# Kernel optimization log

Hardware: AMD Instinct MI355X
Metric: run time of the kernel (lower is better)

Reference implementation:

```python
import jax, jax.numpy as jnp
import numpy as np

N_NODES = 100_000
N_EDGES = 1_000_000
D_IN = 64
D_OUT = 64
N_TYPES = 16  # get_options().in_dim; must exceed gate types 9/11 referenced in source


def setup_inputs() -> dict:
    key = jax.random.key(0)
    k = jax.random.split(key, 6)
    feat = jax.random.normal(k[0], (N_NODES, D_IN), dtype=jnp.float32)
    src = jax.random.randint(k[1], (N_EDGES,), 0, N_NODES, dtype=jnp.int32)
    dst = jax.random.randint(k[2], (N_EDGES,), 0, N_NODES, dtype=jnp.int32)
    ntype2 = jax.random.randint(k[3], (N_NODES,), 0, N_TYPES, dtype=jnp.int32)
    # per-type Linear params; xavier-uniform-ish (gain=sqrt(2) for relu)
    limit = np.sqrt(2.0) * np.sqrt(6.0 / (D_IN + D_OUT))
    gate_W = jax.random.uniform(k[4], (N_TYPES, D_IN, D_OUT), jnp.float32, -limit, limit)
    gate_b = jax.random.uniform(k[5], (N_TYPES, D_OUT), jnp.float32, -0.1, 0.1)
    return {"feat": feat, "gate_W": gate_W, "gate_b": gate_b,
            "src": src, "dst": dst, "ntype2": ntype2, "act_flag": 1}


def reference(feat, gate_W, gate_b, src, dst, ntype2, act_flag):
    n = feat.shape[0]
    # update_all(copy_src('h','m'), mean('m','neigh')): gather + segment-mean
    msg = feat[src]                                                  # [E, D_in]
    summed = jax.ops.segment_sum(msg, dst, num_segments=n)           # [N, D_in]
    deg = jax.ops.segment_sum(jnp.ones_like(dst, dtype=feat.dtype), dst, num_segments=n)
    neigh = summed / jnp.maximum(deg, 1.0)[:, None]                  # zero-degree -> 0 (DGL default)
    # apply_nodes_func: route each node through Linear_t with t = ntype2[node]
    # compute all T small GEMMs, then select per node (T is small and fixed)
    out_all = jnp.einsum('nd,tdo->nto', neigh, gate_W) + gate_b[None, :, :]   # [N, T, D_out]
    rst = jnp.take_along_axis(out_all, ntype2.astype(jnp.int32)[:, None, None], axis=1)[:, 0, :]
    # activation is None in this configuration, so act_flag is a no-op
    return rst
```

## Files before the change

kernel.cpp:

```cpp
#include <hip/hip_runtime.h>

#define N_NODES 100000
#define N_EDGES 1000000
#define D 64
#define N_TYPES 16

#define NPB 128
#define NBUCK ((N_NODES + NPB - 1) / NPB)
#define NBLK 256
#define CHUNK 3908
#define NQUAD (CHUNK / 4)
#define ECAP 1520
#define HCAP 1024

#define AWIN 2048
#define ABLKS ((N_NODES + AWIN - 1) / AWIN)
#define LCAP 256

#define WS_BCUR  0
#define WS_EBUF  (WS_BCUR + NBUCK * 16)
#define WS_TOTAL (WS_EBUF + NBUCK * ECAP + 64)

__device__ __forceinline__ float lane_bcast(float v, int l) {
    return __uint_as_float(__builtin_amdgcn_readlane(__float_as_uint(v), l));
}

__global__ void __launch_bounds__(1024)
place_bucketed(const int* __restrict__ src, const int* __restrict__ dst,
               int* __restrict__ bcur, unsigned* __restrict__ ebuf) {
    __shared__ int hb[NBUCK];
    __shared__ int lo[NBUCK];
    __shared__ int gb[NBUCK];
    __shared__ int cur[NBUCK];
    __shared__ unsigned short stage_bk[CHUNK];
    __shared__ unsigned stage_ls[CHUNK];
    __shared__ int wpart[16];

    int b = blockIdx.x, tid = threadIdx.x;
    int lane = tid & 63, wv = tid >> 6;
    for (int i = tid; i < NBUCK; i += 1024) hb[i] = 0;
    __syncthreads();

    int beg = b * CHUNK;
    int e0 = beg + 4 * tid;
    int4 d4 = make_int4(-1, -1, -1, -1);
    if (tid < NQUAD && e0 < N_EDGES) {
        if (e0 + 3 < N_EDGES) {
            d4 = ((const int4*)(dst + beg))[tid];
        } else {
            d4.x = dst[e0];
            if (e0 + 1 < N_EDGES) d4.y = dst[e0 + 1];
            if (e0 + 2 < N_EDGES) d4.z = dst[e0 + 2];
        }
    }
    if (d4.x >= 0) atomicAdd(&hb[d4.x >> 7], 1);
    if (d4.y >= 0) atomicAdd(&hb[d4.y >> 7], 1);
    if (d4.z >= 0) atomicAdd(&hb[d4.z >> 7], 1);
    if (d4.w >= 0) atomicAdd(&hb[d4.w >> 7], 1);
    __syncthreads();

    int v = (tid < NBUCK) ? hb[tid] : 0;
    int incl = v;
    for (int o = 1; o < 64; o <<= 1) {
        int u = __shfl_up(incl, o, 64);
        if (lane >= o) incl += u;
    }
    if (lane == 63) wpart[wv] = incl;
    __syncthreads();
    if (tid == 0) {
        int r = 0;
        for (int w = 0; w < 16; ++w) { int t = wpart[w]; wpart[w] = r; r += t; }
    }
    __syncthreads();
    incl += wpart[wv];
    int excl = incl - v;
    if (tid < NBUCK) { lo[tid] = excl; cur[tid] = excl; }
    __syncthreads();

    int4 s4 = make_int4(0, 0, 0, 0);
    if (tid < NQUAD && e0 < N_EDGES) {
        if (e0 + 3 < N_EDGES) {
            s4 = ((const int4*)(src + beg))[tid];
        } else {
            s4.x = src[e0];
            if (e0 + 1 < N_EDGES) s4.y = src[e0 + 1];
            if (e0 + 2 < N_EDGES) s4.z = src[e0 + 2];
        }
    }
    if (d4.x >= 0) { int bk = d4.x >> 7; int p = atomicAdd(&cur[bk], 1);
                     stage_bk[p] = (unsigned short)bk;
                     stage_ls[p] = ((unsigned)(d4.x & 127) << 20) | (unsigned)s4.x; }
    if (d4.y >= 0) { int bk = d4.y >> 7; int p = atomicAdd(&cur[bk], 1);
                     stage_bk[p] = (unsigned short)bk;
                     stage_ls[p] = ((unsigned)(d4.y & 127) << 20) | (unsigned)s4.y; }
    if (d4.z >= 0) { int bk = d4.z >> 7; int p = atomicAdd(&cur[bk], 1);
                     stage_bk[p] = (unsigned short)bk;
                     stage_ls[p] = ((unsigned)(d4.z & 127) << 20) | (unsigned)s4.z; }
    if (d4.w >= 0) { int bk = d4.w >> 7; int p = atomicAdd(&cur[bk], 1);
                     stage_bk[p] = (unsigned short)bk;
                     stage_ls[p] = ((unsigned)(d4.w & 127) << 20) | (unsigned)s4.w; }

    if (tid < NBUCK) {
        int c = hb[tid];
        if (c > 0) {
            int base = atomicAdd(&bcur[tid * 16], c);
            gb[tid] = tid * ECAP + base - lo[tid];
        }
    }
    __syncthreads();

    int end = min(beg + CHUNK, N_EDGES);
    int cnt = end - beg;
    for (int idx = tid; idx < cnt; idx += 1024) {
        int bk = (int)stage_bk[idx];
        int p = gb[bk] + idx;
        if ((unsigned)(p - bk * ECAP) < ECAP)
            ebuf[p] = stage_ls[idx];
    }
}

__global__ void __launch_bounds__(256)
bucket_gather(const float* __restrict__ feat, const int* __restrict__ bcur,
              const unsigned* __restrict__ ebuf, float* __restrict__ out) {
    __shared__ int hist[64], offL[64], curL[64];
    __shared__ unsigned eL[ECAP];
    __shared__ int sortedL[HCAP];

    int blk = blockIdx.x, tid = threadIdx.x;
    int bucket = blk >> 1, half = blk & 1;
    int ecnt = bcur[bucket * 16];
    if (ecnt > ECAP) ecnt = ECAP;
    int base = bucket * ECAP;
    if (tid < 64) hist[tid] = 0;
    __syncthreads();

    for (int i = tid; i < ecnt; i += 256) {
        unsigned p = ebuf[base + i];
        eL[i] = p;
        if (((p >> 26) & 1u) == (unsigned)half)
            atomicAdd(&hist[(p >> 20) & 63], 1);
    }
    __syncthreads();
    if (tid < 64) {
        int v = hist[tid];
        int incl = v;
        for (int o = 1; o < 64; o <<= 1) {
            int u = __shfl_up(incl, o, 64);
            if (tid >= o) incl += u;
        }
        offL[tid] = incl - v;
        curL[tid] = incl - v;
    }
    __syncthreads();
    for (int i = tid; i < ecnt; i += 256) {
        unsigned p = eL[i];
        if (((p >> 26) & 1u) == (unsigned)half) {
            int pos = atomicAdd(&curL[(p >> 20) & 63], 1);
            if (pos < HCAP) sortedL[pos] = (int)(p & 0xFFFFFu);
        }
    }
    __syncthreads();

    int hw = tid >> 5, h = tid & 31;
    const float2* __restrict__ F = (const float2*)feat;
    int node0 = bucket * NPB + half * 64;
#pragma unroll
    for (int it = 0; it < 8; ++it) {
        int nl = hw * 8 + it;
        int cnt = hist[nl], o = offL[nl];
        float sx = 0.0f, sy = 0.0f;
        int j = 0;
        for (; j + 4 <= cnt; j += 4) {
            int s0 = sortedL[o + j + 0];
            int s1 = sortedL[o + j + 1];
            int s2 = sortedL[o + j + 2];
            int s3 = sortedL[o + j + 3];
            float2 v0 = F[s0 * 32 + h];
            float2 v1 = F[s1 * 32 + h];
            float2 v2 = F[s2 * 32 + h];
            float2 v3 = F[s3 * 32 + h];
            sx += (v0.x + v1.x) + (v2.x + v3.x);
            sy += (v0.y + v1.y) + (v2.y + v3.y);
        }
        for (; j < cnt; ++j) {
            int s = sortedL[o + j];
            float2 v = F[s * 32 + h];
            sx += v.x; sy += v.y;
        }
        int node = node0 + nl;
        if (node < N_NODES) {
            float scale = (cnt > 1) ? (1.0f / (float)cnt) : 1.0f;
            float2 r; r.x = sx * scale; r.y = sy * scale;
            ((float2*)out)[node * 32 + h] = r;
        }
    }
}

__global__ void __launch_bounds__(512, 2)
type_apply(const float* __restrict__ gate_W, const float* __restrict__ gate_b,
           const int* __restrict__ ntype2, float* __restrict__ out) {
    __shared__ int list[LCAP];
    __shared__ int lcnt;

    int tid = threadIdx.x, lane = tid & 63, wv = tid >> 6;
    int t = blockIdx.x & 15;
    int n0 = (blockIdx.x >> 4) * AWIN;
    if (tid == 0) lcnt = 0;
    __syncthreads();
    for (int i = tid; i < AWIN; i += 512) {
        int n = n0 + i;
        if (n < N_NODES && ntype2[n] == t) {
            int p = atomicAdd(&lcnt, 1);
            if (p < LCAP) list[p] = n;
        }
    }
    __syncthreads();
    int cnt = min(lcnt, LCAP);
    if (cnt == 0) return;

    const float* __restrict__ W = gate_W + t * D * D;
    float wreg[D];
#pragma unroll
    for (int d = 0; d < D; ++d) wreg[d] = W[d * D + lane];
    float bias = gate_b[t * D + lane];

    for (int i = wv; i < cnt; i += 8) {
        int n = list[i];
        float r = out[n * D + lane];
        float a0 = bias, a1 = 0.0f, a2 = 0.0f, a3 = 0.0f;
#pragma unroll
        for (int d = 0; d < D; d += 4) {
            a0 = fmaf(lane_bcast(r, d + 0), wreg[d + 0], a0);
            a1 = fmaf(lane_bcast(r, d + 1), wreg[d + 1], a1);
            a2 = fmaf(lane_bcast(r, d + 2), wreg[d + 2], a2);
            a3 = fmaf(lane_bcast(r, d + 3), wreg[d + 3], a3);
        }
        out[n * D + lane] = (a0 + a1) + (a2 + a3);
    }
}

__global__ void scatter_feat(const float* __restrict__ feat, const int* __restrict__ src,
                             const int* __restrict__ dst, float* __restrict__ accum) {
    long long idx = (long long)blockIdx.x * blockDim.x + threadIdx.x;
    if (idx >= (long long)N_EDGES * D) return;
    int e = (int)(idx >> 6), d = (int)(idx & 63);
    atomicAdd(accum + dst[e] * D + d, feat[src[e] * D + d]);
}
__global__ void scatter_deg(const int* __restrict__ dst, float* __restrict__ deg) {
    int e = blockIdx.x * blockDim.x + threadIdx.x;
    if (e >= N_EDGES) return;
    atomicAdd(deg + dst[e], 1.0f);
}
__global__ void apply_linear(const float* __restrict__ gate_W, const float* __restrict__ gate_b,
                             const int* __restrict__ ntype2, const float* __restrict__ deg,
                             float* __restrict__ out) {
    int node = blockIdx.x * (blockDim.x >> 6) + (threadIdx.x >> 6);
    int lane = threadIdx.x & 63;
    if (node >= N_NODES) return;
    int t = ntype2[node];
    float dv = deg[node]; dv = dv > 1.0f ? dv : 1.0f;
    float nv = out[node * D + lane] / dv;
    const float* W = gate_W + t * D * D;
    float acc = gate_b[t * D + lane];
#pragma unroll 16
    for (int d = 0; d < D; ++d)
        acc = fmaf(__shfl(nv, d, 64), W[d * D + lane], acc);
    out[node * D + lane] = acc;
}

extern "C" void kernel_launch(void* const* d_in, const int* in_sizes, int n_in,
                              void* d_out, int out_size, void* d_ws, size_t ws_size,
                              hipStream_t stream) {
    const float* feat   = (const float*)d_in[0];
    const float* gate_W = (const float*)d_in[1];
    const float* gate_b = (const float*)d_in[2];
    const int*   src    = (const int*)d_in[3];
    const int*   dst    = (const int*)d_in[4];
    const int*   ntype2 = (const int*)d_in[5];
    float* out = (float*)d_out;

    if (ws_size >= (size_t)WS_TOTAL * 4) {
        int* ws = (int*)d_ws;
        int* bcur      = ws + WS_BCUR;
        unsigned* ebuf = (unsigned*)(ws + WS_EBUF);

        hipMemsetAsync(bcur, 0, sizeof(int) * NBUCK * 16, stream);
        place_bucketed<<<NBLK, 1024, 0, stream>>>(src, dst, bcur, ebuf);
        bucket_gather<<<NBUCK * 2, 256, 0, stream>>>(feat, bcur, ebuf, out);
        type_apply<<<ABLKS * 16, 512, 0, stream>>>(gate_W, gate_b, ntype2, out);
    } else {
        float* deg = (float*)d_ws;
        hipMemsetAsync(out, 0, sizeof(float) * N_NODES * D, stream);
        hipMemsetAsync(deg, 0, sizeof(float) * N_NODES, stream);
        long long total = (long long)N_EDGES * D;
        scatter_feat<<<(int)((total + 255) / 256), 256, 0, stream>>>(feat, src, dst, out);
        scatter_deg<<<(N_EDGES + 255) / 256, 256, 0, stream>>>(dst, deg);
        apply_linear<<<(N_NODES + 3) / 4, 256, 0, stream>>>(gate_W, gate_b, ntype2, deg, out);
    }
}
```

Before: 177.0 us.

## Replace atomic bucket reservation with histogram and prefix-scan compact layout

Adds a per-block bucket histogram pass, a column scan over blocks and a bucket-level scan, so that place_bucketed writes edges into a dense, deterministically ordered buffer instead of reserving slots with global atomics in fixed-capacity ECAP buckets. This removes the memset and the contended global atomics, and drops the per-bucket capacity check on writes. In exchange it adds three extra kernel launches and a second read of dst, and the gather still clamps the edge count to ECAP.

```diff
diff --git a/kernel.cpp b/kernel.cpp
--- a/kernel.cpp
+++ b/kernel.cpp
@@ -17,17 +17,69 @@
 #define ABLKS ((N_NODES + AWIN - 1) / AWIN)
 #define LCAP 256
 
-#define WS_BCUR  0
-#define WS_EBUF  (WS_BCUR + NBUCK * 16)
-#define WS_TOTAL (WS_EBUF + NBUCK * ECAP + 64)
+#define WS_TBL    0
+#define WS_BTOT   (WS_TBL + NBUCK * NBLK)
+#define WS_BSTART (WS_BTOT + NBUCK)
+#define WS_EBUF   (WS_BSTART + NBUCK + 1)
+#define WS_TOTAL  (WS_EBUF + N_EDGES + 64)
 
 __device__ __forceinline__ float lane_bcast(float v, int l) {
     return __uint_as_float(__builtin_amdgcn_readlane(__float_as_uint(v), l));
 }
 
+__global__ void __launch_bounds__(256)
+hist_edges(const int* __restrict__ dst, int* __restrict__ tbl) {
+    __shared__ int hb[NBUCK];
+    int b = blockIdx.x, tid = threadIdx.x;
+    for (int i = tid; i < NBUCK; i += 256) hb[i] = 0;
+    __syncthreads();
+    int beg = b * CHUNK, end = min(beg + CHUNK, N_EDGES);
+    for (int e = beg + tid; e < end; e += 256)
+        atomicAdd(&hb[dst[e] >> 7], 1);
+    __syncthreads();
+    for (int i = tid; i < NBUCK; i += 256) tbl[i * NBLK + b] = hb[i];
+}
+
+__global__ void __launch_bounds__(512)
+scan_cols(int* __restrict__ tbl, int* __restrict__ btot) {
+    int wave = blockIdx.x * 8 + (threadIdx.x >> 6);
+    int lane = threadIdx.x & 63;
+    if (wave >= NBUCK) return;
+    int4 v = ((int4*)(tbl + wave * NBLK))[lane];
+    int s01 = v.x + v.y;
+    int s = s01 + v.z + v.w;
+    int incl = s;
+    for (int o = 1; o < 64; o <<= 1) {
+        int u = __shfl_up(incl, o, 64);
+        if (lane >= o) incl += u;
+    }
+    int excl = incl - s;
+    int4 w;
+    w.x = excl; w.y = excl + v.x; w.z = excl + s01; w.w = excl + s01 + v.z;
+    ((int4*)(tbl + wave * NBLK))[lane] = w;
+    if (lane == 63) btot[wave] = incl;
+}
+
+__global__ void __launch_bounds__(1024)
+scan_buckets(const int* __restrict__ btot, int* __restrict__ bstart) {
+    __shared__ int sh[1024];
+    int t = threadIdx.x;
+    int v = (t < NBUCK) ? btot[t] : 0;
+    sh[t] = v;
+    __syncthreads();
+    for (int o = 1; o < 1024; o <<= 1) {
+        int u = (t >= o) ? sh[t - o] : 0;
+        __syncthreads();
+        sh[t] += u;
+        __syncthreads();
+    }
+    if (t <= NBUCK) bstart[t] = sh[t] - v;
+}
+
 __global__ void __launch_bounds__(1024)
 place_bucketed(const int* __restrict__ src, const int* __restrict__ dst,
-               int* __restrict__ bcur, unsigned* __restrict__ ebuf) {
+               const int* __restrict__ tbl, const int* __restrict__ bstart,
+               unsigned* __restrict__ ebuf) {
     __shared__ int hb[NBUCK];
     __shared__ int lo[NBUCK];
     __shared__ int gb[NBUCK];
@@ -100,27 +152,20 @@
                      stage_bk[p] = (unsigned short)bk;
                      stage_ls[p] = ((unsigned)(d4.w & 127) << 20) | (unsigned)s4.w; }
 
-    if (tid < NBUCK) {
-        int c = hb[tid];
-        if (c > 0) {
-            int base = atomicAdd(&bcur[tid * 16], c);
-            gb[tid] = tid * ECAP + base - lo[tid];
-        }
-    }
+    if (tid < NBUCK)
+        gb[tid] = bstart[tid] + tbl[tid * NBLK + b] - lo[tid];
     __syncthreads();
 
     int end = min(beg + CHUNK, N_EDGES);
     int cnt = end - beg;
     for (int idx = tid; idx < cnt; idx += 1024) {
         int bk = (int)stage_bk[idx];
-        int p = gb[bk] + idx;
-        if ((unsigned)(p - bk * ECAP) < ECAP)
-            ebuf[p] = stage_ls[idx];
+        ebuf[gb[bk] + idx] = stage_ls[idx];
     }
 }
 
 __global__ void __launch_bounds__(256)
-bucket_gather(const float* __restrict__ feat, const int* __restrict__ bcur,
+bucket_gather(const float* __restrict__ feat, const int* __restrict__ bstart,
               const unsigned* __restrict__ ebuf, float* __restrict__ out) {
     __shared__ int hist[64], offL[64], curL[64];
     __shared__ unsigned eL[ECAP];
@@ -128,9 +173,9 @@
 
     int blk = blockIdx.x, tid = threadIdx.x;
     int bucket = blk >> 1, half = blk & 1;
-    int ecnt = bcur[bucket * 16];
+    int base = bstart[bucket];
+    int ecnt = bstart[bucket + 1] - base;
     if (ecnt > ECAP) ecnt = ECAP;
-    int base = bucket * ECAP;
     if (tid < 64) hist[tid] = 0;
     __syncthreads();
 
@@ -281,12 +326,16 @@
 
     if (ws_size >= (size_t)WS_TOTAL * 4) {
         int* ws = (int*)d_ws;
-        int* bcur      = ws + WS_BCUR;
+        int* tbl       = ws + WS_TBL;
+        int* btot      = ws + WS_BTOT;
+        int* bstart    = ws + WS_BSTART;
         unsigned* ebuf = (unsigned*)(ws + WS_EBUF);
 
-        hipMemsetAsync(bcur, 0, sizeof(int) * NBUCK * 16, stream);
-        place_bucketed<<<NBLK, 1024, 0, stream>>>(src, dst, bcur, ebuf);
-        bucket_gather<<<NBUCK * 2, 256, 0, stream>>>(feat, bcur, ebuf, out);
+        hist_edges<<<NBLK, 256, 0, stream>>>(dst, tbl);
+        scan_cols<<<(NBUCK + 7) / 8, 512, 0, stream>>>(tbl, btot);
+        scan_buckets<<<1, 1024, 0, stream>>>(btot, bstart);
+        place_bucketed<<<NBLK, 1024, 0, stream>>>(src, dst, tbl, bstart, ebuf);
+        bucket_gather<<<NBUCK * 2, 256, 0, stream>>>(feat, bstart, ebuf, out);
         type_apply<<<ABLKS * 16, 512, 0, stream>>>(gate_W, gate_b, ntype2, out);
     } else {
         float* deg = (float*)d_ws;
```

Result: no change. 176.4 us (-0.3%).
